# Performance work log

Measured on AMD Instinct MI355X. Metric: run time of the kernel, lower is better.

Reference implementation:

```python
import jax, jax.numpy as jnp
import numpy as np

C = 2.3026  # Poincare ball curvature
EPS = 1e-15

def _hlinear(x, z, r, c):
    # hypll-style Poincare fully connected layer (HNN++, Shimizu et al.)
    # x: (B, fi) on ball, z: (fi, fo), r: (fo,)
    cs = jnp.sqrt(c)
    lam = 2.0 / (1.0 - c * jnp.sum(x * x, axis=-1, keepdims=True))  # conformal factor (B,1)
    zn = jnp.maximum(jnp.sqrt(jnp.sum(z * z, axis=0)), EPS)         # (fo,)
    tcr = 2.0 * cs * r                                              # (fo,)
    # signed hyperplane distances v_k
    d = (2.0 * zn / cs) * jnp.arcsinh(
        cs * lam * (x @ z) / zn * jnp.cosh(tcr) - (lam - 1.0) * jnp.sinh(tcr))
    w = jnp.sinh(cs * d) / cs
    # map back into the ball: ||out|| < 1/sqrt(c)
    return w / (1.0 + jnp.sqrt(1.0 + c * jnp.sum(w * w, axis=-1, keepdims=True)))

def _hrelu(x, c):
    # logmap at origin -> ReLU in tangent space -> expmap at origin
    cs = jnp.sqrt(c)
    n = jnp.maximum(jnp.sqrt(jnp.sum(x * x, axis=-1, keepdims=True)), EPS)
    v = jnp.arctanh(jnp.minimum(cs * n, 1.0 - 1e-7)) * x / (cs * n)
    v = jax.nn.relu(v)
    vn = jnp.maximum(jnp.sqrt(jnp.sum(v * v, axis=-1, keepdims=True)), EPS)
    return jnp.tanh(cs * vn) * v / (cs * vn)

def setup_inputs() -> dict:
    key = jax.random.key(0)
    ks = jax.random.split(key, 9)
    B, D = 65536, 768
    xs = 0.02 * jax.random.normal(ks[0], (B, D), dtype=jnp.float32)
    # repo preprocessing: lift to Lorentz (K=C) then Lorentz->Poincare
    x0 = jnp.sqrt(1.0 / C + jnp.sum(xs * xs, axis=-1, keepdims=True))
    x = xs / (x0 + 1.0)  # strictly inside ball of radius 1/sqrt(C)
    def mk(k, fi, fo):
        return (jax.random.normal(k, (fi, fo), dtype=jnp.float32) / np.float32(np.sqrt(fi)))
    return {
        "x": x,
        "z1": mk(ks[1], 768, 512), "b1": 0.01 * jax.random.normal(ks[2], (512,), dtype=jnp.float32),
        "z2": mk(ks[3], 512, 256), "b2": 0.01 * jax.random.normal(ks[4], (256,), dtype=jnp.float32),
        "z3": mk(ks[5], 256, 128), "b3": 0.01 * jax.random.normal(ks[6], (128,), dtype=jnp.float32),
        "z4": mk(ks[7], 128, 1),   "b4": 0.01 * jax.random.normal(ks[8], (1,), dtype=jnp.float32),
    }

def reference(x, z1, b1, z2, b2, z3, b3, z4, b4):
    h = _hrelu(_hlinear(x, z1, b1, C), C)
    h = _hrelu(_hlinear(h, z2, b2, C), C)
    h = _hrelu(_hlinear(h, z3, b3, C), C)
    return _hlinear(h, z4, b4, C)
```

## Files before the change

### kernel.cpp

```cpp
#include <hip/hip_runtime.h>

#define CURV 2.3026f
#define EPSF 1e-15f

typedef __attribute__((ext_vector_type(8))) short bfrag8;
typedef __attribute__((ext_vector_type(4))) float ffrag4;

static __device__ __forceinline__ unsigned short f2bf(float f) {
  unsigned u = __builtin_bit_cast(unsigned, f);
  u += 0x7fffu + ((u >> 16) & 1u);
  return (unsigned short)(u >> 16);
}

static __device__ __forceinline__ void gld16(const void* g, void* l) {
  unsigned lo = (unsigned)(unsigned long long)l;
  __builtin_amdgcn_global_load_lds(
      (const __attribute__((address_space(1))) unsigned int*)g,
      (__attribute__((address_space(3))) unsigned int*)lo, 16, 0, 0);
}

__global__ void prep_all(const float* __restrict__ z1, const float* __restrict__ r1,
                         const float* __restrict__ z2, const float* __restrict__ r2,
                         const float* __restrict__ z3, const float* __restrict__ r3,
                         const float* __restrict__ z4, const float* __restrict__ r4,
                         unsigned short* __restrict__ zT1, float* __restrict__ st1,
                         unsigned short* __restrict__ zT2, float* __restrict__ st2,
                         unsigned short* __restrict__ zT3, float* __restrict__ st3,
                         unsigned short* __restrict__ zT4, float* __restrict__ st4) {
  int b = blockIdx.x, t = threadIdx.x;
  const float *z, *r; unsigned short* zT; float* st; int K, N, n;
  if (b < 512)      { z = z1; r = r1; zT = zT1; st = st1; K = 768; N = 512; n = b; }
  else if (b < 768) { z = z2; r = r2; zT = zT2; st = st2; K = 512; N = 256; n = b - 512; }
  else if (b < 896) { z = z3; r = r3; zT = zT3; st = st3; K = 256; N = 128; n = b - 768; }
  else              { z = z4; r = r4; zT = zT4; st = st4; K = 128; N = 1;   n = 0; }
  float ss = 0.f;
  for (int k = t; k < K; k += 128) {
    float v = z[(size_t)k * N + n];
    ss += v * v;
    zT[(size_t)n * K + k] = f2bf(v);
  }
  __shared__ float red[128];
  red[t] = ss; __syncthreads();
  for (int s = 64; s > 0; s >>= 1) { if (t < s) red[t] += red[t + s]; __syncthreads(); }
  if (t == 0) {
    float zn = fmaxf(sqrtf(red[0]), EPSF);
    float cs = sqrtf(CURV);
    float tc = 2.f * cs * r[n];
    st[4*n+0] = 2.f * (zn - 1.f);
    st[4*n+1] = coshf(tc) / zn;
    st[4*n+2] = sinhf(tc);
    st[4*n+3] = 0.f;
  }
}

template<int NT>
static __device__ __forceinline__ void poly_w(ffrag4 (&acc)[2][NT], const float* __restrict__ stats,
                                              int wn, int lm, int wm, int quad,
                                              const float* lamP, float cs, float inv_cs) {
#pragma unroll
  for (int tn = 0; tn < NT; tn++) {
    float4 st = *(const float4*)(stats + 4 * (wn * (16 * NT) + 16 * tn + lm));
    float dl = st.x, chozn = st.y, sh = st.z;
#pragma unroll
    for (int tm = 0; tm < 2; tm++) {
#pragma unroll
      for (int rg = 0; rg < 4; rg++) {
        float lam = lamP[32 * wm + 16 * tm + 4 * quad + rg];
        float g = cs * lam * acc[tm][tn][rg] * chozn - (lam - 1.f) * sh;
        float q = g * g;
        float u = g * (1.f - q * (1.f / 6.f) + q * q * 0.075f - q * q * q * 0.044642857f);
        float d1 = dl * u;
        float S = 2.f * g * sqrtf(1.f + q);
        float Ch = 1.f + 2.f * q;
        acc[tm][tn][rg] = (S * (1.f + 0.5f * d1 * d1) + Ch * d1) * inv_cs;
      }
    }
  }
}

template<int NT, bool L4>
static __device__ __forceinline__ void reduce_rows(ffrag4 (&acc)[2][NT], const float* z4v,
                                                   int lm, int wm, int quad, float (*sums_)[64]) {
#pragma unroll
  for (int tm = 0; tm < 2; tm++) {
#pragma unroll
    for (int rg = 0; rg < 4; rg++) {
      float s2 = 0.f, sp2 = 0.f, s4 = 0.f;
#pragma unroll
      for (int tn = 0; tn < NT; tn++) {
        float w = acc[tm][tn][rg];
        s2 += w * w;
        float wp = fmaxf(w, 0.f);
        sp2 += wp * wp;
        if (L4) s4 += wp * z4v[tn];
      }
#pragma unroll
      for (int m = 1; m <= 8; m <<= 1) {
        s2 += __shfl_xor(s2, m, 16);
        sp2 += __shfl_xor(sp2, m, 16);
        if (L4) s4 += __shfl_xor(s4, m, 16);
      }
      if (lm == 0) {
        int row = 32 * wm + 16 * tm + 4 * quad + rg;
        atomicAdd(&sums_[0][row], s2);
        atomicAdd(&sums_[1][row], sp2);
        if (L4) atomicAdd(&sums_[2][row], s4);
      }
    }
  }
}

template<int NT>
static __device__ __forceinline__ void panel_write(ffrag4 (&acc)[2][NT], char* panel,
                                                   int lm, int wm, int wn, int quad,
                                                   const float* gamP) {
#pragma unroll
  for (int tm = 0; tm < 2; tm++)
#pragma unroll
    for (int rg = 0; rg < 4; rg++) {
      const int r = 32 * wm + 16 * tm + 4 * quad + rg;
      const float gam = gamP[r];
      const unsigned rb = (unsigned)((r >> 1) * 128);
      const unsigned rx = (unsigned)((r >> 1) & 7);
      const unsigned c0 = (unsigned)((r & 1) * 4);
#pragma unroll
      for (int tn = 0; tn < NT; tn++) {
        const int col = wn * (16 * NT) + 16 * tn + lm;
        const unsigned ad = (unsigned)((col >> 5) * 4096) + rb +
                            (((c0 + (unsigned)((col >> 3) & 3)) ^ rx) << 4) +
                            (unsigned)((col & 7) * 2);
        *(unsigned short*)(panel + ad) = f2bf(gam * fmaxf(acc[tm][tn][rg], 0.f));
      }
    }
}

static __device__ __forceinline__ float stage_a4(float4 f, char* p) {
  ushort4 h; h.x = f2bf(f.x); h.y = f2bf(f.y); h.z = f2bf(f.z); h.w = f2bf(f.w);
  *(ushort4*)p = h;
  return f.x * f.x + f.y * f.y + f.z * f.z + f.w * f.w;
}

__launch_bounds__(1024, 4)
__global__ void fused_mlp(const float* __restrict__ x,
                          const unsigned short* __restrict__ zt1, const float* __restrict__ st1,
                          const unsigned short* __restrict__ zt2, const float* __restrict__ st2,
                          const unsigned short* __restrict__ zt3, const float* __restrict__ st3,
                          const float* __restrict__ z4, const float* __restrict__ st4,
                          float* __restrict__ outF) {
  __shared__ __align__(16) char smem[147456];
  __shared__ float lamS[64];
  __shared__ float gamS[64];
  __shared__ float sums[3][64];

  const int t = threadIdx.x;
  const int wid = t >> 6, lane = t & 63;
  const int wm = wid >> 3, wn = wid & 7;
  const int lm = lane & 15, quad = lane >> 4;
  const int l7 = lane & 7, rl8 = lane >> 3;
  const unsigned rowg0 = blockIdx.x * 64u;

  char* const A1 = smem;
  char* const B1 = smem + 16384;
  char* const H1 = smem;
  char* const B2 = smem + 65536;
  char* const H2 = smem;
  char* const B3 = smem + 32768;

  const unsigned cB = (unsigned)(l7 ^ rl8);
  const unsigned ldst = (unsigned)(lane * 16);

  const unsigned sl16 = (unsigned)(((((lm & 1) << 2) + quad) ^ (lm >> 1)) << 4);
  unsigned afoff[2];
#pragma unroll
  for (int tm = 0; tm < 2; tm++) afoff[tm] = (unsigned)((16 * wm + 8 * tm + (lm >> 1)) * 128) + sl16;
  unsigned bf1off[4];
#pragma unroll
  for (int tn = 0; tn < 4; tn++) bf1off[tn] = (unsigned)((wn * 32 + 8 * tn + (lm >> 1)) * 128) + sl16;
  unsigned bf2off[2];
#pragma unroll
  for (int tn = 0; tn < 2; tn++) bf2off[tn] = (unsigned)((wn * 16 + 8 * tn + (lm >> 1)) * 128) + sl16;
  const unsigned bf3off = (unsigned)((wn * 8 + (lm >> 1)) * 128) + sl16;

  const int mrow = 4 * wid + (lane >> 4);
  const unsigned kloc = 4u * (unsigned)(lane & 15);
  const char* a1g = (const char*)x + (size_t)(rowg0 + (unsigned)mrow) * 3072 + kloc * 4u;
  const unsigned kk = kloc & 31u;
  const unsigned a1d = (kloc >> 5) * 4096u + (unsigned)(mrow >> 1) * 128u +
                       ((((unsigned)(mrow & 1) * 4u + (kk >> 3)) ^ ((unsigned)(mrow >> 1) & 7u)) << 4) +
                       ((kk >> 2) & 1u) * 8u;

  unsigned b1s[4], b1d[4];
#pragma unroll
  for (int j = 0; j < 4; j++) {
    unsigned rr = (unsigned)(wid + 16 * j);
    unsigned R = 8u * (rr & 31u) + (unsigned)rl8;
    unsigned n = 2u * R + (cB >> 2);
    b1s[j] = n * 1536u + (rr >> 5) * 64u + (cB & 3u) * 16u;
    b1d[j] = rr * 1024u + ldst;
  }
  unsigned b2s[2], b2d[2];
#pragma unroll
  for (int j = 0; j < 2; j++) {
    unsigned rr = (unsigned)(wid + 16 * j);
    unsigned R = 8u * (rr & 15u) + (unsigned)rl8;
    unsigned n = 2u * R + (cB >> 2);
    b2s[j] = n * 1024u + (rr >> 4) * 64u + (cB & 3u) * 16u;
    b2d[j] = rr * 1024u + ldst;
  }
  unsigned b3s, b3d;
  {
    unsigned rr = (unsigned)wid;
    unsigned R = 8u * (rr & 7u) + (unsigned)rl8;
    unsigned n = 2u * R + (cB >> 2);
    b3s = n * 512u + (rr >> 3) * 64u + (cB & 3u) * 16u;
    b3d = rr * 1024u + ldst;
  }

  float ss = 0.f;
  {
    float4 p0 = *(const float4*)a1g;
    ss += stage_a4(p0, A1 + a1d);
  }
  float4 pA = *(const float4*)(a1g + 256);
#pragma unroll
  for (int j = 0; j < 4; j++) gld16((const char*)zt1 + b1s[j], B1 + b1d[j]);

  ffrag4 acc1[2][4];
#pragma unroll
  for (int a = 0; a < 2; a++)
#pragma unroll
    for (int b = 0; b < 4; b++) acc1[a][b] = (ffrag4){0.f, 0.f, 0.f, 0.f};

  for (int k = 0; k < 12; k++) {
    __syncthreads();
    char* curA = A1 + (k & 1) * 8192;
    char* curB = B1 + (k & 1) * 65536;
    if (k < 11) {
      char* nA = A1 + ((k + 1) & 1) * 8192;
      char* nB = B1 + ((k + 1) & 1) * 65536;
      unsigned adv = (unsigned)(k + 1) * 128u;
#pragma unroll
      for (int j = 0; j < 4; j++) gld16((const char*)zt1 + b1s[j] + adv, nB + b1d[j]);
      ss += stage_a4(pA, nA + a1d);
      if (k < 10) pA = *(const float4*)(a1g + (size_t)(k + 2) * 256);
    }
#pragma unroll
    for (int kt = 0; kt < 2; kt++) {
      bfrag8 a0 = *(const bfrag8*)(curA + kt * 4096 + afoff[0]);
      bfrag8 a1f = *(const bfrag8*)(curA + kt * 4096 + afoff[1]);
#pragma unroll
      for (int tn = 0; tn < 4; tn++) {
        bfrag8 bf = *(const bfrag8*)(curB + kt * 32768 + bf1off[tn]);
        acc1[0][tn] = __builtin_amdgcn_mfma_f32_16x16x32_bf16(a0, bf, acc1[0][tn], 0, 0, 0);
        acc1[1][tn] = __builtin_amdgcn_mfma_f32_16x16x32_bf16(a1f, bf, acc1[1][tn], 0, 0, 0);
      }
    }
  }

  __syncthreads();
#pragma unroll
  for (int j = 0; j < 2; j++) gld16((const char*)zt2 + b2s[j], B2 + b2d[j]);

  ss += __shfl_xor(ss, 1); ss += __shfl_xor(ss, 2);
  ss += __shfl_xor(ss, 4); ss += __shfl_xor(ss, 8);
  if ((lane & 15) == 0) lamS[mrow] = 2.f / (1.f - CURV * ss);
  if (t < 64) { sums[0][t] = 0.f; sums[1][t] = 0.f; }
  __syncthreads();

  const float cs = sqrtf(CURV), inv_cs = 1.f / cs;
  poly_w<4>(acc1, st1, wn, lm, wm, quad, lamS, cs, inv_cs);
  reduce_rows<4, false>(acc1, nullptr, lm, wm, quad, sums);
  __syncthreads();
  if (t < 64) {
    float sw2 = sums[0][t], swp2 = sums[1][t];
    float den = 1.f + sqrtf(1.f + CURV * sw2);
    float nn = fmaxf(sqrtf(sw2) / den, EPSF);
    float al = atanhf(fminf(cs * nn, 1.f - 1e-7f)) / (cs * nn);
    float vn = fmaxf(al * sqrtf(swp2) / den, EPSF);
    float be = tanhf(cs * vn) / (cs * vn);
    float gam = al * be / den;
    gamS[t] = gam;
    lamS[t] = 2.f / (1.f - CURV * gam * gam * swp2);
  }
  __syncthreads();
  panel_write<4>(acc1, H1, lm, wm, wn, quad, gamS);
  if (t < 64) { sums[0][t] = 0.f; sums[1][t] = 0.f; }

  ffrag4 acc2[2][2];
#pragma unroll
  for (int a = 0; a < 2; a++)
#pragma unroll
    for (int b = 0; b < 2; b++) acc2[a][b] = (ffrag4){0.f, 0.f, 0.f, 0.f};

  for (int k = 0; k < 8; k++) {
    __syncthreads();
    char* curB = B2 + (k & 1) * 32768;
    if (k < 7) {
      char* nB = B2 + ((k + 1) & 1) * 32768;
      unsigned adv = (unsigned)(k + 1) * 128u;
#pragma unroll
      for (int j = 0; j < 2; j++) gld16((const char*)zt2 + b2s[j] + adv, nB + b2d[j]);
    }
#pragma unroll
    for (int kt = 0; kt < 2; kt++) {
      bfrag8 a0 = *(const bfrag8*)(H1 + (2 * k + kt) * 4096 + afoff[0]);
      bfrag8 a1f = *(const bfrag8*)(H1 + (2 * k + kt) * 4096 + afoff[1]);
#pragma unroll
      for (int tn = 0; tn < 2; tn++) {
        bfrag8 bf = *(const bfrag8*)(curB + kt * 16384 + bf2off[tn]);
        acc2[0][tn] = __builtin_amdgcn_mfma_f32_16x16x32_bf16(a0, bf, acc2[0][tn], 0, 0, 0);
        acc2[1][tn] = __builtin_amdgcn_mfma_f32_16x16x32_bf16(a1f, bf, acc2[1][tn], 0, 0, 0);
      }
    }
  }

  __syncthreads();
  gld16((const char*)zt3 + b3s, B3 + b3d);
  poly_w<2>(acc2, st2, wn, lm, wm, quad, lamS, cs, inv_cs);
  reduce_rows<2, false>(acc2, nullptr, lm, wm, quad, sums);
  __syncthreads();
  if (t < 64) {
    float sw2 = sums[0][t], swp2 = sums[1][t];
    float den = 1.f + sqrtf(1.f + CURV * sw2);
    float nn = fmaxf(sqrtf(sw2) / den, EPSF);
    float al = atanhf(fminf(cs * nn, 1.f - 1e-7f)) / (cs * nn);
    float vn = fmaxf(al * sqrtf(swp2) / den, EPSF);
    float be = tanhf(cs * vn) / (cs * vn);
    float gam = al * be / den;
    gamS[t] = gam;
    lamS[t] = 2.f / (1.f - CURV * gam * gam * swp2);
  }
  __syncthreads();
  panel_write<2>(acc2, H2, lm, wm, wn, quad, gamS);
  if (t < 64) { sums[0][t] = 0.f; sums[1][t] = 0.f; sums[2][t] = 0.f; }

  ffrag4 acc3[2][1];
  acc3[0][0] = (ffrag4){0.f, 0.f, 0.f, 0.f};
  acc3[1][0] = (ffrag4){0.f, 0.f, 0.f, 0.f};
  float z4v[1] = { z4[wn * 16 + lm] };

  for (int k = 0; k < 4; k++) {
    __syncthreads();
    char* curB = B3 + (k & 1) * 16384;
    if (k < 3)
      gld16((const char*)zt3 + b3s + (unsigned)(k + 1) * 128u,
            B3 + ((k + 1) & 1) * 16384 + b3d);
#pragma unroll
    for (int kt = 0; kt < 2; kt++) {
      bfrag8 a0 = *(const bfrag8*)(H2 + (2 * k + kt) * 4096 + afoff[0]);
      bfrag8 a1f = *(const bfrag8*)(H2 + (2 * k + kt) * 4096 + afoff[1]);
      bfrag8 bf = *(const bfrag8*)(curB + kt * 8192 + bf3off);
      acc3[0][0] = __builtin_amdgcn_mfma_f32_16x16x32_bf16(a0, bf, acc3[0][0], 0, 0, 0);
      acc3[1][0] = __builtin_amdgcn_mfma_f32_16x16x32_bf16(a1f, bf, acc3[1][0], 0, 0, 0);
    }
  }
  __syncthreads();

  poly_w<1>(acc3, st3, wn, lm, wm, quad, lamS, cs, inv_cs);
  reduce_rows<1, true>(acc3, z4v, lm, wm, quad, sums);
  __syncthreads();
  if (t < 64) {
    float sw2 = sums[0][t], swp2 = sums[1][t];
    float den = 1.f + sqrtf(1.f + CURV * sw2);
    float nn = fmaxf(sqrtf(sw2) / den, EPSF);
    float al = atanhf(fminf(cs * nn, 1.f - 1e-7f)) / (cs * nn);
    float vn = fmaxf(al * sqrtf(swp2) / den, EPSF);
    float be = tanhf(cs * vn) / (cs * vn);
    float gam = al * be / den;
    float s = gam * sums[2][t];
    float lamh = 2.f / (1.f - CURV * gam * gam * swp2);
    float g = cs * lamh * s * st4[1] - (lamh - 1.f) * st4[2];
    float q = g * g;
    float u = g * (1.f - q * (1.f / 6.f) + q * q * 0.075f - q * q * q * 0.044642857f);
    float d1 = st4[0] * u;
    float S = 2.f * g * sqrtf(1.f + q);
    float Ch = 1.f + 2.f * q;
    float w = (S * (1.f + 0.5f * d1 * d1) + Ch * d1) * inv_cs;
    outF[rowg0 + t] = w / (1.f + sqrtf(1.f + CURV * w * w));
  }
}

extern "C" void kernel_launch(void* const* d_in, const int* in_sizes, int n_in,
                              void* d_out, int out_size, void* d_ws, size_t ws_size,
                              hipStream_t stream) {
  const float* x  = (const float*)d_in[0];
  const float* z1 = (const float*)d_in[1];
  const float* b1 = (const float*)d_in[2];
  const float* z2 = (const float*)d_in[3];
  const float* b2 = (const float*)d_in[4];
  const float* z3 = (const float*)d_in[5];
  const float* b3 = (const float*)d_in[6];
  const float* z4 = (const float*)d_in[7];
  const float* b4 = (const float*)d_in[8];

  char* ws = (char*)d_ws; size_t off = 0;
  auto carve = [&](size_t b) { char* p = ws + off; off += (b + 255) & ~(size_t)255; return p; };
  unsigned short* zT1 = (unsigned short*)carve(512 * 768 * 2);
  unsigned short* zT2 = (unsigned short*)carve(256 * 512 * 2);
  unsigned short* zT3 = (unsigned short*)carve(128 * 256 * 2);
  unsigned short* zT4 = (unsigned short*)carve(128 * 2);
  float* st1 = (float*)carve(512 * 4 * 4);
  float* st2 = (float*)carve(256 * 4 * 4);
  float* st3 = (float*)carve(128 * 4 * 4);
  float* st4 = (float*)carve(4 * 4);

  prep_all<<<897, 128, 0, stream>>>(z1, b1, z2, b2, z3, b3, z4, b4,
                                    zT1, st1, zT2, st2, zT3, st3, zT4, st4);
  fused_mlp<<<1024, 1024, 0, stream>>>(x, zT1, st1, zT2, st2, zT3, st3, z4, st4, (float*)d_out);
}
```

Before: 450.9 us.

## Halve fused MLP shared memory, read layer 2/3 weights from global, tile prep

Cuts the fused kernel's LDS from 144KB to 72KB by halving the layer-1 K step to 32 and dropping the LDS staging of layer-2/3 weights. Those weights are now read directly from global memory (L2-resident) into MFMA fragments. The goal is to fit two 1024-thread blocks per CU and raise occupancy, at the cost of more layer-1 iterations and barriers and uncached global fragment loads. The weight prep kernel is also rewritten to transpose through an LDS tile, using 15 blocks with coalesced writes.

```diff
diff --git a/kernel.cpp b/kernel.cpp
--- a/kernel.cpp
+++ b/kernel.cpp
@@ -19,37 +19,68 @@
       (__attribute__((address_space(3))) unsigned int*)lo, 16, 0, 0);
 }
 
-__global__ void prep_all(const float* __restrict__ z1, const float* __restrict__ r1,
-                         const float* __restrict__ z2, const float* __restrict__ r2,
-                         const float* __restrict__ z3, const float* __restrict__ r3,
-                         const float* __restrict__ z4, const float* __restrict__ r4,
-                         unsigned short* __restrict__ zT1, float* __restrict__ st1,
-                         unsigned short* __restrict__ zT2, float* __restrict__ st2,
-                         unsigned short* __restrict__ zT3, float* __restrict__ st3,
-                         unsigned short* __restrict__ zT4, float* __restrict__ st4) {
+__global__ void prep_tiled(const float* __restrict__ z1, const float* __restrict__ r1,
+                           const float* __restrict__ z2, const float* __restrict__ r2,
+                           const float* __restrict__ z3, const float* __restrict__ r3,
+                           const float* __restrict__ z4, const float* __restrict__ r4,
+                           unsigned short* __restrict__ zT1, float* __restrict__ st1,
+                           unsigned short* __restrict__ zT2, float* __restrict__ st2,
+                           unsigned short* __restrict__ zT3, float* __restrict__ st3,
+                           unsigned short* __restrict__ zT4, float* __restrict__ st4) {
   int b = blockIdx.x, t = threadIdx.x;
-  const float *z, *r; unsigned short* zT; float* st; int K, N, n;
-  if (b < 512)      { z = z1; r = r1; zT = zT1; st = st1; K = 768; N = 512; n = b; }
-  else if (b < 768) { z = z2; r = r2; zT = zT2; st = st2; K = 512; N = 256; n = b - 512; }
-  else if (b < 896) { z = z3; r = r3; zT = zT3; st = st3; K = 256; N = 128; n = b - 768; }
-  else              { z = z4; r = r4; zT = zT4; st = st4; K = 128; N = 1;   n = 0; }
-  float ss = 0.f;
-  for (int k = t; k < K; k += 128) {
-    float v = z[(size_t)k * N + n];
-    ss += v * v;
-    zT[(size_t)n * K + k] = f2bf(v);
-  }
-  __shared__ float red[128];
-  red[t] = ss; __syncthreads();
-  for (int s = 64; s > 0; s >>= 1) { if (t < s) red[t] += red[t + s]; __syncthreads(); }
-  if (t == 0) {
-    float zn = fmaxf(sqrtf(red[0]), EPSF);
-    float cs = sqrtf(CURV);
-    float tc = 2.f * cs * r[n];
-    st[4*n+0] = 2.f * (zn - 1.f);
-    st[4*n+1] = coshf(tc) / zn;
-    st[4*n+2] = sinhf(tc);
-    st[4*n+3] = 0.f;
+  const float *z, *rv; unsigned short* zT; float* st; int K, N, nt;
+  if (b < 8)       { z = z1; rv = r1; zT = zT1; st = st1; K = 768; N = 512; nt = b; }
+  else if (b < 12) { z = z2; rv = r2; zT = zT2; st = st2; K = 512; N = 256; nt = b - 8; }
+  else if (b < 14) { z = z3; rv = r3; zT = zT3; st = st3; K = 256; N = 128; nt = b - 12; }
+  else             { z = z4; rv = r4; zT = zT4; st = st4; K = 128; N = 1;   nt = 0; }
+  const float cs = sqrtf(CURV);
+  if (N == 1) {
+    float v = (t < K) ? z[t] : 0.f;
+    if (t < K) zT[t] = f2bf(v);
+    float ssl = v * v;
+    __shared__ float red4[4];
+    for (int m = 1; m <= 32; m <<= 1) ssl += __shfl_xor(ssl, m);
+    if ((t & 63) == 0) red4[t >> 6] = ssl;
+    __syncthreads();
+    if (t == 0) {
+      float ss = red4[0] + red4[1] + red4[2] + red4[3];
+      float zn = fmaxf(sqrtf(ss), EPSF);
+      float tc = 2.f * cs * rv[0];
+      st[0] = 2.f * (zn - 1.f); st[1] = coshf(tc) / zn; st[2] = sinhf(tc); st[3] = 0.f;
+    }
+    return;
+  }
+  __shared__ unsigned short tile[64 * 72];
+  __shared__ float red[4][64];
+  const int c = t & 63, rq = t >> 6;
+  const int n0 = nt * 64;
+  float ssl = 0.f;
+  for (int kk = 0; kk < K; kk += 64) {
+#pragma unroll
+    for (int p = 0; p < 16; p++) {
+      int k = kk + 4 * p + rq;
+      float v = z[(size_t)k * N + n0 + c];
+      ssl += v * v;
+      tile[c * 72 + 4 * p + rq] = f2bf(v);
+    }
+    __syncthreads();
+    {
+      int wr = t >> 2, seg = t & 3;
+      const unsigned long long* src = (const unsigned long long*)(tile + wr * 72 + seg * 16);
+      unsigned long long* dst = (unsigned long long*)(zT + (size_t)(n0 + wr) * K + kk + seg * 16);
+      dst[0] = src[0]; dst[1] = src[1]; dst[2] = src[2]; dst[3] = src[3];
+    }
+    __syncthreads();
+  }
+  red[rq][c] = ssl; __syncthreads();
+  if (t < 64) {
+    float ss = red[0][t] + red[1][t] + red[2][t] + red[3][t];
+    float zn = fmaxf(sqrtf(ss), EPSF);
+    float tc = 2.f * cs * rv[n0 + t];
+    st[4 * (n0 + t) + 0] = 2.f * (zn - 1.f);
+    st[4 * (n0 + t) + 1] = coshf(tc) / zn;
+    st[4 * (n0 + t) + 2] = sinhf(tc);
+    st[4 * (n0 + t) + 3] = 0.f;
   }
 }
 
@@ -134,20 +165,20 @@
     }
 }
 
-static __device__ __forceinline__ float stage_a4(float4 f, char* p) {
-  ushort4 h; h.x = f2bf(f.x); h.y = f2bf(f.y); h.z = f2bf(f.z); h.w = f2bf(f.w);
-  *(ushort4*)p = h;
-  return f.x * f.x + f.y * f.y + f.z * f.z + f.w * f.w;
-}
-
-__launch_bounds__(1024, 4)
+static __device__ __forceinline__ float stage_a2(float2 f, char* p) {
+  unsigned lo = f2bf(f.x), hi = f2bf(f.y);
+  *(unsigned*)p = lo | (hi << 16);
+  return f.x * f.x + f.y * f.y;
+}
+
+__launch_bounds__(1024, 8)
 __global__ void fused_mlp(const float* __restrict__ x,
                           const unsigned short* __restrict__ zt1, const float* __restrict__ st1,
                           const unsigned short* __restrict__ zt2, const float* __restrict__ st2,
                           const unsigned short* __restrict__ zt3, const float* __restrict__ st3,
                           const float* __restrict__ z4, const float* __restrict__ st4,
                           float* __restrict__ outF) {
-  __shared__ __align__(16) char smem[147456];
+  __shared__ __align__(16) char smem[73728];
   __shared__ float lamS[64];
   __shared__ float gamS[64];
   __shared__ float sums[3][64];
@@ -160,14 +191,11 @@
   const unsigned rowg0 = blockIdx.x * 64u;
 
   char* const A1 = smem;
-  char* const B1 = smem + 16384;
+  char* const B1 = smem + 8192;
   char* const H1 = smem;
-  char* const B2 = smem + 65536;
   char* const H2 = smem;
-  char* const B3 = smem + 32768;
 
   const unsigned cB = (unsigned)(l7 ^ rl8);
-  const unsigned ldst = (unsigned)(lane * 16);
 
   const unsigned sl16 = (unsigned)(((((lm & 1) << 2) + quad) ^ (lm >> 1)) << 4);
   unsigned afoff[2];
@@ -176,54 +204,30 @@
   unsigned bf1off[4];
 #pragma unroll
   for (int tn = 0; tn < 4; tn++) bf1off[tn] = (unsigned)((wn * 32 + 8 * tn + (lm >> 1)) * 128) + sl16;
-  unsigned bf2off[2];
-#pragma unroll
-  for (int tn = 0; tn < 2; tn++) bf2off[tn] = (unsigned)((wn * 16 + 8 * tn + (lm >> 1)) * 128) + sl16;
-  const unsigned bf3off = (unsigned)((wn * 8 + (lm >> 1)) * 128) + sl16;
-
-  const int mrow = 4 * wid + (lane >> 4);
-  const unsigned kloc = 4u * (unsigned)(lane & 15);
-  const char* a1g = (const char*)x + (size_t)(rowg0 + (unsigned)mrow) * 3072 + kloc * 4u;
-  const unsigned kk = kloc & 31u;
-  const unsigned a1d = (kloc >> 5) * 4096u + (unsigned)(mrow >> 1) * 128u +
-                       ((((unsigned)(mrow & 1) * 4u + (kk >> 3)) ^ ((unsigned)(mrow >> 1) & 7u)) << 4) +
-                       ((kk >> 2) & 1u) * 8u;
-
-  unsigned b1s[4], b1d[4];
-#pragma unroll
-  for (int j = 0; j < 4; j++) {
-    unsigned rr = (unsigned)(wid + 16 * j);
-    unsigned R = 8u * (rr & 31u) + (unsigned)rl8;
-    unsigned n = 2u * R + (cB >> 2);
-    b1s[j] = n * 1536u + (rr >> 5) * 64u + (cB & 3u) * 16u;
-    b1d[j] = rr * 1024u + ldst;
-  }
-  unsigned b2s[2], b2d[2];
+
+  const int mrow = 4 * wid + quad;
+  const char* a1g = (const char*)x + (size_t)(rowg0 + (unsigned)mrow) * 3072 + (size_t)lm * 8;
+  const unsigned a1d = (unsigned)(mrow >> 1) * 128u +
+                       ((((unsigned)(mrow & 1) * 4u + ((unsigned)lm >> 2)) ^ ((unsigned)(mrow >> 1) & 7u)) << 4) +
+                       ((unsigned)lm & 3u) * 4u;
+
+  unsigned b1s[2], b1d[2];
 #pragma unroll
   for (int j = 0; j < 2; j++) {
     unsigned rr = (unsigned)(wid + 16 * j);
-    unsigned R = 8u * (rr & 15u) + (unsigned)rl8;
-    unsigned n = 2u * R + (cB >> 2);
-    b2s[j] = n * 1024u + (rr >> 4) * 64u + (cB & 3u) * 16u;
-    b2d[j] = rr * 1024u + ldst;
-  }
-  unsigned b3s, b3d;
-  {
-    unsigned rr = (unsigned)wid;
-    unsigned R = 8u * (rr & 7u) + (unsigned)rl8;
-    unsigned n = 2u * R + (cB >> 2);
-    b3s = n * 512u + (rr >> 3) * 64u + (cB & 3u) * 16u;
-    b3d = rr * 1024u + ldst;
+    unsigned N_ = 16u * rr + 2u * (unsigned)rl8 + (cB >> 2);
+    b1s[j] = N_ * 1536u + (cB & 3u) * 16u;
+    b1d[j] = rr * 1024u + (unsigned)lane * 16u;
   }
 
   float ss = 0.f;
   {
-    float4 p0 = *(const float4*)a1g;
-    ss += stage_a4(p0, A1 + a1d);
-  }
-  float4 pA = *(const float4*)(a1g + 256);
-#pragma unroll
-  for (int j = 0; j < 4; j++) gld16((const char*)zt1 + b1s[j], B1 + b1d[j]);
+    float2 p0 = *(const float2*)a1g;
+    ss += stage_a2(p0, A1 + a1d);
+  }
+  float2 pA = *(const float2*)(a1g + 128);
+  gld16((const char*)zt1 + b1s[0], B1 + b1d[0]);
+  gld16((const char*)zt1 + b1s[1], B1 + b1d[1]);
 
   ffrag4 acc1[2][4];
 #pragma unroll
@@ -231,39 +235,34 @@
 #pragma unroll
     for (int b = 0; b < 4; b++) acc1[a][b] = (ffrag4){0.f, 0.f, 0.f, 0.f};
 
-  for (int k = 0; k < 12; k++) {
+  for (int k = 0; k < 24; k++) {
     __syncthreads();
-    char* curA = A1 + (k & 1) * 8192;
-    char* curB = B1 + (k & 1) * 65536;
-    if (k < 11) {
-      char* nA = A1 + ((k + 1) & 1) * 8192;
-      char* nB = B1 + ((k + 1) & 1) * 65536;
-      unsigned adv = (unsigned)(k + 1) * 128u;
-#pragma unroll
-      for (int j = 0; j < 4; j++) gld16((const char*)zt1 + b1s[j] + adv, nB + b1d[j]);
-      ss += stage_a4(pA, nA + a1d);
-      if (k < 10) pA = *(const float4*)(a1g + (size_t)(k + 2) * 256);
-    }
-#pragma unroll
-    for (int kt = 0; kt < 2; kt++) {
-      bfrag8 a0 = *(const bfrag8*)(curA + kt * 4096 + afoff[0]);
-      bfrag8 a1f = *(const bfrag8*)(curA + kt * 4096 + afoff[1]);
-#pragma unroll
-      for (int tn = 0; tn < 4; tn++) {
-        bfrag8 bf = *(const bfrag8*)(curB + kt * 32768 + bf1off[tn]);
-        acc1[0][tn] = __builtin_amdgcn_mfma_f32_16x16x32_bf16(a0, bf, acc1[0][tn], 0, 0, 0);
-        acc1[1][tn] = __builtin_amdgcn_mfma_f32_16x16x32_bf16(a1f, bf, acc1[1][tn], 0, 0, 0);
-      }
-    }
-  }
-
-  __syncthreads();
-#pragma unroll
-  for (int j = 0; j < 2; j++) gld16((const char*)zt2 + b2s[j], B2 + b2d[j]);
+    char* curA = A1 + (k & 1) * 4096;
+    char* curB = B1 + (k & 1) * 32768;
+    if (k < 23) {
+      char* nA = A1 + ((k + 1) & 1) * 4096;
+      char* nB = B1 + ((k + 1) & 1) * 32768;
+      unsigned adv = (unsigned)(k + 1) * 64u;
+      gld16((const char*)zt1 + b1s[0] + adv, nB + b1d[0]);
+      gld16((const char*)zt1 + b1s[1] + adv, nB + b1d[1]);
+      ss += stage_a2(pA, nA + a1d);
+      if (k < 22) pA = *(const float2*)(a1g + (size_t)(k + 2) * 128);
+    }
+    bfrag8 a0 = *(const bfrag8*)(curA + afoff[0]);
+    bfrag8 a1f = *(const bfrag8*)(curA + afoff[1]);
+#pragma unroll
+    for (int tn = 0; tn < 4; tn++) {
+      bfrag8 bf = *(const bfrag8*)(curB + bf1off[tn]);
+      acc1[0][tn] = __builtin_amdgcn_mfma_f32_16x16x32_bf16(a0, bf, acc1[0][tn], 0, 0, 0);
+      acc1[1][tn] = __builtin_amdgcn_mfma_f32_16x16x32_bf16(a1f, bf, acc1[1][tn], 0, 0, 0);
+    }
+  }
+
+  __syncthreads();
 
   ss += __shfl_xor(ss, 1); ss += __shfl_xor(ss, 2);
   ss += __shfl_xor(ss, 4); ss += __shfl_xor(ss, 8);
-  if ((lane & 15) == 0) lamS[mrow] = 2.f / (1.f - CURV * ss);
+  if (lm == 0) lamS[mrow] = 2.f / (1.f - CURV * ss);
   if (t < 64) { sums[0][t] = 0.f; sums[1][t] = 0.f; }
   __syncthreads();
 
@@ -281,10 +280,11 @@
     float gam = al * be / den;
     gamS[t] = gam;
     lamS[t] = 2.f / (1.f - CURV * gam * gam * swp2);
+    sums[0][t] = 0.f; sums[1][t] = 0.f;
   }
   __syncthreads();
   panel_write<4>(acc1, H1, lm, wm, wn, quad, gamS);
-  if (t < 64) { sums[0][t] = 0.f; sums[1][t] = 0.f; }
+  __syncthreads();
 
   ffrag4 acc2[2][2];
 #pragma unroll
@@ -292,30 +292,20 @@
 #pragma unroll
     for (int b = 0; b < 2; b++) acc2[a][b] = (ffrag4){0.f, 0.f, 0.f, 0.f};
 
-  for (int k = 0; k < 8; k++) {
-    __syncthreads();
-    char* curB = B2 + (k & 1) * 32768;
-    if (k < 7) {
-      char* nB = B2 + ((k + 1) & 1) * 32768;
-      unsigned adv = (unsigned)(k + 1) * 128u;
-#pragma unroll
-      for (int j = 0; j < 2; j++) gld16((const char*)zt2 + b2s[j] + adv, nB + b2d[j]);
-    }
-#pragma unroll
-    for (int kt = 0; kt < 2; kt++) {
-      bfrag8 a0 = *(const bfrag8*)(H1 + (2 * k + kt) * 4096 + afoff[0]);
-      bfrag8 a1f = *(const bfrag8*)(H1 + (2 * k + kt) * 4096 + afoff[1]);
-#pragma unroll
-      for (int tn = 0; tn < 2; tn++) {
-        bfrag8 bf = *(const bfrag8*)(curB + kt * 16384 + bf2off[tn]);
-        acc2[0][tn] = __builtin_amdgcn_mfma_f32_16x16x32_bf16(a0, bf, acc2[0][tn], 0, 0, 0);
-        acc2[1][tn] = __builtin_amdgcn_mfma_f32_16x16x32_bf16(a1f, bf, acc2[1][tn], 0, 0, 0);
-      }
-    }
-  }
-
-  __syncthreads();
-  gld16((const char*)zt3 + b3s, B3 + b3d);
+  const char* b2base = (const char*)zt2 + (size_t)(32 * wn + lm) * 1024 + (size_t)quad * 16;
+#pragma unroll 4
+  for (int kt = 0; kt < 16; kt++) {
+    bfrag8 b0 = *(const bfrag8*)(b2base + kt * 64);
+    bfrag8 b1v = *(const bfrag8*)(b2base + 16384 + kt * 64);
+    bfrag8 a0 = *(const bfrag8*)(H1 + kt * 4096 + afoff[0]);
+    bfrag8 a1f = *(const bfrag8*)(H1 + kt * 4096 + afoff[1]);
+    acc2[0][0] = __builtin_amdgcn_mfma_f32_16x16x32_bf16(a0,  b0,  acc2[0][0], 0, 0, 0);
+    acc2[0][1] = __builtin_amdgcn_mfma_f32_16x16x32_bf16(a0,  b1v, acc2[0][1], 0, 0, 0);
+    acc2[1][0] = __builtin_amdgcn_mfma_f32_16x16x32_bf16(a1f, b0,  acc2[1][0], 0, 0, 0);
+    acc2[1][1] = __builtin_amdgcn_mfma_f32_16x16x32_bf16(a1f, b1v, acc2[1][1], 0, 0, 0);
+  }
+  __syncthreads();
+
   poly_w<2>(acc2, st2, wn, lm, wm, quad, lamS, cs, inv_cs);
   reduce_rows<2, false>(acc2, nullptr, lm, wm, quad, sums);
   __syncthreads();
@@ -329,32 +319,26 @@
     float gam = al * be / den;
     gamS[t] = gam;
     lamS[t] = 2.f / (1.f - CURV * gam * gam * swp2);
+    sums[0][t] = 0.f; sums[1][t] = 0.f; sums[2][t] = 0.f;
   }
   __syncthreads();
   panel_write<2>(acc2, H2, lm, wm, wn, quad, gamS);
-  if (t < 64) { sums[0][t] = 0.f; sums[1][t] = 0.f; sums[2][t] = 0.f; }
+  __syncthreads();
 
   ffrag4 acc3[2][1];
   acc3[0][0] = (ffrag4){0.f, 0.f, 0.f, 0.f};
   acc3[1][0] = (ffrag4){0.f, 0.f, 0.f, 0.f};
   float z4v[1] = { z4[wn * 16 + lm] };
 
-  for (int k = 0; k < 4; k++) {
-    __syncthreads();
-    char* curB = B3 + (k & 1) * 16384;
-    if (k < 3)
-      gld16((const char*)zt3 + b3s + (unsigned)(k + 1) * 128u,
-            B3 + ((k + 1) & 1) * 16384 + b3d);
-#pragma unroll
-    for (int kt = 0; kt < 2; kt++) {
-      bfrag8 a0 = *(const bfrag8*)(H2 + (2 * k + kt) * 4096 + afoff[0]);
-      bfrag8 a1f = *(const bfrag8*)(H2 + (2 * k + kt) * 4096 + afoff[1]);
-      bfrag8 bf = *(const bfrag8*)(curB + kt * 8192 + bf3off);
-      acc3[0][0] = __builtin_amdgcn_mfma_f32_16x16x32_bf16(a0, bf, acc3[0][0], 0, 0, 0);
-      acc3[1][0] = __builtin_amdgcn_mfma_f32_16x16x32_bf16(a1f, bf, acc3[1][0], 0, 0, 0);
-    }
-  }
-  __syncthreads();
+  const char* b3base = (const char*)zt3 + (size_t)(16 * wn + lm) * 512 + (size_t)quad * 16;
+#pragma unroll 4
+  for (int kt = 0; kt < 8; kt++) {
+    bfrag8 bf = *(const bfrag8*)(b3base + kt * 64);
+    bfrag8 a0 = *(const bfrag8*)(H2 + kt * 4096 + afoff[0]);
+    bfrag8 a1f = *(const bfrag8*)(H2 + kt * 4096 + afoff[1]);
+    acc3[0][0] = __builtin_amdgcn_mfma_f32_16x16x32_bf16(a0,  bf, acc3[0][0], 0, 0, 0);
+    acc3[1][0] = __builtin_amdgcn_mfma_f32_16x16x32_bf16(a1f, bf, acc3[1][0], 0, 0, 0);
+  }
 
   poly_w<1>(acc3, st3, wn, lm, wm, quad, lamS, cs, inv_cs);
   reduce_rows<1, true>(acc3, z4v, lm, wm, quad, sums);
@@ -404,7 +388,7 @@
   float* st3 = (float*)carve(128 * 4 * 4);
   float* st4 = (float*)carve(4 * 4);
 
-  prep_all<<<897, 128, 0, stream>>>(z1, b1, z2, b2, z3, b3, z4, b4,
-                                    zT1, st1, zT2, st2, zT3, st3, zT4, st4);
+  prep_tiled<<<15, 256, 0, stream>>>(z1, b1, z2, b2, z3, b3, z4, b4,
+                                     zT1, st1, zT2, st2, zT3, st3, zT4, st4);
   fused_mlp<<<1024, 1024, 0, stream>>>(x, zT1, st1, zT2, st2, zT3, st3, z4, st4, (float*)d_out);
 }
```

Result: slower. 506.5 us (+12.3%).
